# Kernel tuning notes

Measured on AMD Instinct MI355X. Metric: run time of the kernel, lower is better.

## Reference

```python
import jax, jax.numpy as jnp
import numpy as np

B, S, D, H = 8, 1024, 512, 8
HD = D // H
EPS = 1e-5


def layer_norm(x, g, b):
    m = jnp.mean(x, axis=-1, keepdims=True)
    v = jnp.mean(jnp.square(x - m), axis=-1, keepdims=True)
    return (x - m) * jax.lax.rsqrt(v + EPS) * g + b


def mha(x, w_in, b_in, w_out, b_out):
    # x: [B,S,D]; w_in: [3D,D]; PyTorch MultiheadAttention math (no dropout, eval)
    b, s, d = x.shape
    qkv = x @ w_in.T + b_in                      # [B,S,3D]
    q, k, v = jnp.split(qkv, 3, axis=-1)
    q = q.reshape(b, s, H, HD)
    k = k.reshape(b, s, H, HD)
    v = v.reshape(b, s, H, HD)
    scores = jnp.einsum('bqhd,bkhd->bhqk', q, k) / np.sqrt(HD)
    a = jax.nn.softmax(scores, axis=-1)
    o = jnp.einsum('bhqk,bkhd->bqhd', a, v).reshape(b, s, d)
    return o @ w_out.T + b_out


def interp_linear(y, out_size):
    # y: [B,S_in,D]; torch F.interpolate(mode='linear', align_corners=False)
    s_in = y.shape[1]
    scale = s_in / out_size
    src = (jnp.arange(out_size, dtype=jnp.float32) + 0.5) * scale - 0.5
    src = jnp.clip(src, 0.0, s_in - 1.0)
    i0 = jnp.floor(src).astype(jnp.int32)
    i1 = jnp.minimum(i0 + 1, s_in - 1)
    w = (src - i0.astype(jnp.float32))[None, :, None]
    return y[:, i0, :] * (1.0 - w) + y[:, i1, :] * w


def setup_inputs() -> dict:
    key = jax.random.key(0)
    ks = jax.random.split(key, 16)
    sd = 0.02
    return {
        'x': jax.random.normal(ks[0], (B, S, D), jnp.float32),
        'w_in1': jax.random.normal(ks[1], (3 * D, D), jnp.float32) * sd,
        'b_in1': jnp.zeros((3 * D,), jnp.float32),
        'w_out1': jax.random.normal(ks[2], (D, D), jnp.float32) * sd,
        'b_out1': jnp.zeros((D,), jnp.float32),
        'w_in2': jax.random.normal(ks[3], (3 * D, D), jnp.float32) * sd,
        'b_in2': jnp.zeros((3 * D,), jnp.float32),
        'w_out2': jax.random.normal(ks[4], (D, D), jnp.float32) * sd,
        'b_out2': jnp.zeros((D,), jnp.float32),
        'g1': jnp.ones((D,), jnp.float32), 'beta1': jnp.zeros((D,), jnp.float32),
        'g2': jnp.ones((D,), jnp.float32), 'beta2': jnp.zeros((D,), jnp.float32),
        'g3': jnp.ones((D,), jnp.float32), 'beta3': jnp.zeros((D,), jnp.float32),
        'w_ff1': jax.random.normal(ks[5], (4 * D, D), jnp.float32) * sd,
        'b_ff1': jnp.zeros((4 * D,), jnp.float32),
        'w_ff2': jax.random.normal(ks[6], (D, 4 * D), jnp.float32) * sd,
        'b_ff2': jnp.zeros((D,), jnp.float32),
    }


def reference(x, w_in1, b_in1, w_out1, b_out1, w_in2, b_in2, w_out2, b_out2,
              g1, beta1, g2, beta2, g3, beta3, w_ff1, b_ff1, w_ff2, b_ff2):
    a1 = mha(x, w_in1, b_in1, w_out1, b_out1)
    x = layer_norm(x + a1, g1, beta1)
    # avg_pool1d kernel=2 stride=2 ceil_mode (S even -> exact halving)
    pooled = x.reshape(B, S // 2, 2, D).mean(axis=2)
    a2 = mha(pooled, w_in2, b_in2, w_out2, b_out2)
    up = interp_linear(a2, S)
    x = layer_norm(x + up, g2, beta2)
    h = jax.nn.gelu(x @ w_ff1.T + b_ff1, approximate=False)
    ff = h @ w_ff2.T + b_ff2
    return layer_norm(x + ff, g3, beta3)
```

## Files before the change

### kernel.cpp

```cpp
#include <hip/hip_runtime.h>
#include <hip/hip_bf16.h>
#include <math.h>

typedef __hip_bfloat16 bf16;
typedef __attribute__((ext_vector_type(8))) short short8;
typedef __attribute__((ext_vector_type(4))) short s4v;
typedef __attribute__((ext_vector_type(4))) float f32x4;

__device__ __forceinline__ float ldf(const float* p, size_t i) { return p[i]; }
__device__ __forceinline__ float ldf(const bf16*  p, size_t i) { return __bfloat162float(p[i]); }
__device__ __forceinline__ void  stf(float* p, size_t i, float v) { p[i] = v; }
__device__ __forceinline__ void  stf(bf16*  p, size_t i, float v) { p[i] = __float2bfloat16(v); }

__device__ __forceinline__ float ex2(float x) { return __builtin_amdgcn_exp2f(x); }

__device__ __forceinline__ void gl16(const void* gp, void* lp) {
    __builtin_amdgcn_global_load_lds(
        (const __attribute__((address_space(1))) void*)gp,
        (__attribute__((address_space(3))) void*)lp, 16, 0, 0);
}

__global__ __launch_bounds__(256) void cvt_kernel(
    const float* __restrict__ src, bf16* __restrict__ dst, int n)
{
    for (int i = blockIdx.x * 256 + threadIdx.x; i < n; i += gridDim.x * 256)
        dst[i] = __float2bfloat16(src[i]);
}

__global__ __launch_bounds__(256) void cvt_w(
    const float* __restrict__ s0, const float* __restrict__ s1,
    const float* __restrict__ s2, const float* __restrict__ s3,
    const float* __restrict__ s4, const float* __restrict__ s5,
    bf16* __restrict__ dst)
{
    int i = blockIdx.x * 256 + threadIdx.x;
    const float* s; int off;
    if      (i <  786432) { s = s0; off = 0; }
    else if (i < 1048576) { s = s1; off =  786432; }
    else if (i < 1835008) { s = s2; off = 1048576; }
    else if (i < 2097152) { s = s3; off = 1835008; }
    else if (i < 3145728) { s = s4; off = 2097152; }
    else                  { s = s5; off = 3145728; }
    dst[i] = __float2bfloat16(s[i - off]);
}

template <int EPI>
__global__ __launch_bounds__(256) void gemm_mfma(
    const bf16* __restrict__ A, const bf16* __restrict__ W,
    const float* __restrict__ bias, bf16* __restrict__ C,
    int M, int N, int K)
{
    __shared__ __align__(16) bf16 Asl[2][128 * 64];
    __shared__ __align__(16) bf16 Bsl[2][128 * 64];

    const int tid  = threadIdx.x;
    const int lane = tid & 63;
    const int wave = tid >> 6;
    const int wm   = wave >> 1;
    const int wn   = wave & 1;
    const int l15  = lane & 15;
    const int quad = lane >> 4;
    const int sr   = lane >> 3;
    const int sc   = ((lane & 7) ^ sr) * 8;

    const int row0 = blockIdx.y * 128, col0 = blockIdx.x * 128;

    f32x4 acc[4][4] = {};

    const int nk = K >> 6;

    #pragma unroll
    for (int t = 0; t < 4; t++) {
        int r0 = wave * 32 + t * 8;
        gl16(&A[(size_t)(row0 + r0 + sr) * K + sc], &Asl[0][r0 * 64]);
        gl16(&W[(size_t)(col0 + r0 + sr) * K + sc], &Bsl[0][r0 * 64]);
    }

    int cur = 0;
    for (int i = 0; i < nk; i++) {
        __syncthreads();
        if (i + 1 < nk) {
            int k1 = (i + 1) << 6;
            #pragma unroll
            for (int t = 0; t < 4; t++) {
                int r0 = wave * 32 + t * 8;
                gl16(&A[(size_t)(row0 + r0 + sr) * K + k1 + sc], &Asl[cur ^ 1][r0 * 64]);
                gl16(&W[(size_t)(col0 + r0 + sr) * K + k1 + sc], &Bsl[cur ^ 1][r0 * 64]);
            }
        }

        #pragma unroll
        for (int ks = 0; ks < 64; ks += 32) {
            short8 af[4], bfr[4];
            const int g0 = (ks >> 3) + quad;
            const int col = (g0 ^ (l15 & 7)) * 8;
            #pragma unroll
            for (int mt = 0; mt < 4; mt++)
                af[mt] = *(const short8*)&Asl[cur][(wm * 64 + mt * 16 + l15) * 64 + col];
            #pragma unroll
            for (int nt = 0; nt < 4; nt++)
                bfr[nt] = *(const short8*)&Bsl[cur][(wn * 64 + nt * 16 + l15) * 64 + col];
            #pragma unroll
            for (int mt = 0; mt < 4; mt++)
                #pragma unroll
                for (int nt = 0; nt < 4; nt++)
                    acc[mt][nt] = __builtin_amdgcn_mfma_f32_16x16x32_bf16(
                        af[mt], bfr[nt], acc[mt][nt], 0, 0, 0);
        }
        cur ^= 1;
    }

    #pragma unroll
    for (int mt = 0; mt < 4; mt++) {
        int row = row0 + wm * 64 + mt * 16 + quad * 4;
        #pragma unroll
        for (int nt = 0; nt < 4; nt++) {
            int col = col0 + wn * 64 + nt * 16 + l15;
            float bv = bias[col];
            #pragma unroll
            for (int r = 0; r < 4; r++) {
                float v = acc[mt][nt][r] + bv;
                if (EPI == 1) v = 0.5f * v * (1.0f + erff(v * 0.70710678118654752f));
                C[(size_t)(row + r) * N + col] = __float2bfloat16(v);
            }
        }
    }
}

template <int LQ>
__global__ __launch_bounds__(256) void flash_attn_mfma(
    const bf16* __restrict__ qkv, bf16* __restrict__ o)
{
    __shared__ __align__(16) bf16 Ks[64 * 72];
    __shared__ __align__(16) bf16 Vt[64 * 68];
    __shared__ __align__(16) bf16 Pl[4][16 * 72];

    const int S   = 64 << LQ;
    const int nQB = 1 << LQ;

    const int tid  = threadIdx.x;
    const int wave = tid >> 6, lane = tid & 63;
    const int l15  = lane & 15, quad = lane >> 4;

    const int r    = blockIdx.x;
    const int w    = (r & 7) * (8 << LQ) + (r >> 3);
    const int qblk = w & (nQB - 1);
    const int bh   = w >> LQ;
    const int h    = bh & 7, bb = bh >> 3;
    const int q0   = qblk * 64;

    const bf16* base = qkv + (size_t)bb * S * 1536 + h * 64;

    short8 qf[2];
    {
        size_t qoff = (size_t)(q0 + wave * 16 + l15) * 1536;
        qf[0] = *(const short8*)&base[qoff + quad * 8];
        qf[1] = *(const short8*)&base[qoff + 32 + quad * 8];
    }

    f32x4 oacc[4] = {};
    float m2 = -3.0e38f, lrow = 0.f;
    const float CE = 0.18033688f;

    short8 kst[2];
    s4v    vst[4];
    const int vr4 = (tid >> 4) * 4;
    const int vc0 = (tid & 15) * 4;

    auto LOADK = [&](int k0) {
        #pragma unroll
        for (int t = 0; t < 2; t++) {
            int c = tid + 256 * t;
            int rr = c >> 3, col = (c & 7) * 8;
            kst[t] = *(const short8*)&base[(size_t)(k0 + rr) * 1536 + 512 + col];
        }
        #pragma unroll
        for (int rr = 0; rr < 4; rr++)
            vst[rr] = *(const s4v*)&base[(size_t)(k0 + vr4 + rr) * 1536 + 1024 + vc0];
    };

    auto WRITEKV = [&]() {
        #pragma unroll
        for (int t = 0; t < 2; t++) {
            int c = tid + 256 * t;
            int rr = c >> 3, col = (c & 7) * 8;
            *(short8*)&Ks[rr * 72 + col] = kst[t];
        }
        #pragma unroll
        for (int i = 0; i < 4; i++) {
            union { bf16 b[4]; unsigned u[2]; } pk;
            pk.b[0] = ((const bf16*)&vst[0])[i];
            pk.b[1] = ((const bf16*)&vst[1])[i];
            pk.b[2] = ((const bf16*)&vst[2])[i];
            pk.b[3] = ((const bf16*)&vst[3])[i];
            *(unsigned long long*)&Vt[(vc0 + i) * 68 + vr4] =
                *(const unsigned long long*)pk.u;
        }
    };

    LOADK(0);
    const int nt = 1 << LQ;
    for (int it = 0; it < nt; it++) {
        __syncthreads();
        WRITEKV();
        __syncthreads();
        if (it + 1 < nt) LOADK((it + 1) << 6);

        f32x4 st[4] = {};
        #pragma unroll
        for (int mt = 0; mt < 4; mt++) {
            short8 kf0 = *(const short8*)&Ks[(mt * 16 + l15) * 72 + quad * 8];
            short8 kf1 = *(const short8*)&Ks[(mt * 16 + l15) * 72 + 32 + quad * 8];
            st[mt] = __builtin_amdgcn_mfma_f32_16x16x32_bf16(kf0, qf[0], st[mt], 0, 0, 0);
            st[mt] = __builtin_amdgcn_mfma_f32_16x16x32_bf16(kf1, qf[1], st[mt], 0, 0, 0);
        }

        float cm = -3.0e38f;
        #pragma unroll
        for (int mt = 0; mt < 4; mt++)
            #pragma unroll
            for (int rr = 0; rr < 4; rr++) cm = fmaxf(cm, st[mt][rr]);
        cm = fmaxf(cm, __shfl_xor(cm, 16));
        cm = fmaxf(cm, __shfl_xor(cm, 32));
        float cm2 = cm * CE;

        if (__any(cm2 > m2 + 8.f)) {
            float mn2   = fmaxf(m2, cm2);
            float alpha = ex2(m2 - mn2);
            m2 = mn2;
            lrow *= alpha;
            float a4[4];
            #pragma unroll
            for (int rr = 0; rr < 4; rr++) a4[rr] = __shfl(alpha, quad * 4 + rr);
            #pragma unroll
            for (int ntt = 0; ntt < 4; ntt++)
                #pragma unroll
                for (int rr = 0; rr < 4; rr++) oacc[ntt][rr] *= a4[rr];
        }

        float ps = 0.f;
        #pragma unroll
        for (int mt = 0; mt < 4; mt++) {
            s4v pw;
            #pragma unroll
            for (int rr = 0; rr < 4; rr++) {
                float p = ex2(st[mt][rr] * CE - m2);
                ps += p;
                union { bf16 b; short hh; } cv;
                cv.b = __float2bfloat16(p);
                pw[rr] = cv.hh;
            }
            *(s4v*)&Pl[wave][l15 * 72 + mt * 16 + quad * 4] = pw;
        }
        ps += __shfl_xor(ps, 16);
        ps += __shfl_xor(ps, 32);
        lrow += ps;

        #pragma unroll
        for (int kb = 0; kb < 2; kb++) {
            short8 pf = *(const short8*)&Pl[wave][l15 * 72 + kb * 32 + quad * 8];
            #pragma unroll
            for (int ntt = 0; ntt < 4; ntt++) {
                const bf16* vp = &Vt[(ntt * 16 + l15) * 68 + kb * 32 + quad * 8];
                short8 vf;
                *(unsigned long long*)&vf       = *(const unsigned long long*)vp;
                *((unsigned long long*)&vf + 1) = *(const unsigned long long*)(vp + 4);
                oacc[ntt] = __builtin_amdgcn_mfma_f32_16x16x32_bf16(pf, vf, oacc[ntt], 0, 0, 0);
            }
        }
    }

    float inv = 1.0f / lrow;
    float iv[4];
    #pragma unroll
    for (int rr = 0; rr < 4; rr++) iv[rr] = __shfl(inv, quad * 4 + rr);
    #pragma unroll
    for (int ntt = 0; ntt < 4; ntt++)
        #pragma unroll
        for (int rr = 0; rr < 4; rr++) {
            size_t row = (size_t)bb * S + q0 + wave * 16 + quad * 4 + rr;
            o[row * 512 + h * 64 + ntt * 16 + l15] = __float2bfloat16(oacc[ntt][rr] * iv[rr]);
        }
}

template <typename AT, typename OT, bool INTERP>
__global__ __launch_bounds__(256) void ln_kernel(
    const AT* __restrict__ a, const bf16* __restrict__ bsrc,
    const float* __restrict__ g, const float* __restrict__ beta,
    OT* __restrict__ out)
{
    const int row = blockIdx.x;
    const int t = threadIdx.x;
    const size_t base = (size_t)row * 512;

    float a0 = ldf(a, base + t), a1 = ldf(a, base + t + 256);
    float b0, b1;
    if (INTERP) {
        int s = row & 1023, bb = row >> 10;
        float src = fminf(fmaxf((s + 0.5f) * 0.5f - 0.5f, 0.f), 511.f);
        int i0 = (int)src;
        int i1 = min(i0 + 1, 511);
        float w = src - (float)i0;
        size_t r0 = ((size_t)bb * 512 + i0) * 512;
        size_t r1 = ((size_t)bb * 512 + i1) * 512;
        b0 = __bfloat162float(bsrc[r0 + t]) * (1.f - w) + __bfloat162float(bsrc[r1 + t]) * w;
        b1 = __bfloat162float(bsrc[r0 + t + 256]) * (1.f - w) + __bfloat162float(bsrc[r1 + t + 256]) * w;
    } else {
        b0 = __bfloat162float(bsrc[base + t]);
        b1 = __bfloat162float(bsrc[base + t + 256]);
    }
    float v0 = a0 + b0, v1 = a1 + b1;

    __shared__ float red[4];
    const int lane = t & 63, wid = t >> 6;

    float sm = v0 + v1;
    #pragma unroll
    for (int off = 32; off > 0; off >>= 1) sm += __shfl_xor(sm, off);
    if (lane == 0) red[wid] = sm;
    __syncthreads();
    sm = red[0] + red[1] + red[2] + red[3];
    const float mean = sm * (1.0f / 512.0f);

    float d0 = v0 - mean, d1 = v1 - mean;
    float vv = d0 * d0 + d1 * d1;
    __syncthreads();
    #pragma unroll
    for (int off = 32; off > 0; off >>= 1) vv += __shfl_xor(vv, off);
    if (lane == 0) red[wid] = vv;
    __syncthreads();
    vv = red[0] + red[1] + red[2] + red[3];
    const float rstd = rsqrtf(vv * (1.0f / 512.0f) + 1e-5f);

    stf(out, base + t,       d0 * rstd * g[t]       + beta[t]);
    stf(out, base + t + 256, d1 * rstd * g[t + 256] + beta[t + 256]);
}

__global__ __launch_bounds__(256) void pool_kernel(
    const bf16* __restrict__ x, bf16* __restrict__ p)
{
    size_t i = (size_t)blockIdx.x * 256 + threadIdx.x;
    size_t d = i & 511;
    size_t rs = i >> 9;
    size_t b = rs >> 9, s = rs & 511;
    size_t r = (b * 1024 + 2 * s) * 512 + d;
    p[i] = __float2bfloat16(0.5f * (__bfloat162float(x[r]) + __bfloat162float(x[r + 512])));
}

extern "C" void kernel_launch(void* const* d_in, const int* in_sizes, int n_in,
                              void* d_out, int out_size, void* d_ws, size_t ws_size,
                              hipStream_t stream)
{
    const float* x      = (const float*)d_in[0];
    const float* w_in1  = (const float*)d_in[1];
    const float* b_in1  = (const float*)d_in[2];
    const float* w_out1 = (const float*)d_in[3];
    const float* b_out1 = (const float*)d_in[4];
    const float* w_in2  = (const float*)d_in[5];
    const float* b_in2  = (const float*)d_in[6];
    const float* w_out2 = (const float*)d_in[7];
    const float* b_out2 = (const float*)d_in[8];
    const float* g1     = (const float*)d_in[9];
    const float* be1    = (const float*)d_in[10];
    const float* g2     = (const float*)d_in[11];
    const float* be2    = (const float*)d_in[12];
    const float* g3     = (const float*)d_in[13];
    const float* be3    = (const float*)d_in[14];
    const float* w_ff1  = (const float*)d_in[15];
    const float* b_ff1  = (const float*)d_in[16];
    const float* w_ff2  = (const float*)d_in[17];
    const float* b_ff2  = (const float*)d_in[18];

    bf16* ws     = (bf16*)d_ws;
    bf16* xb     = ws + 0;
    bf16* wq1    = ws + 4194304;
    bf16* wo1    = ws + 4980736;
    bf16* wq2    = ws + 5242880;
    bf16* wo2    = ws + 6029312;
    bf16* wf1    = ws + 6291456;
    bf16* wf2    = ws + 7340032;
    bf16* qkv1   = ws + 8388608;
    bf16* o1     = ws + 20971520;
    bf16* a1     = ws + 25165824;
    bf16* x1     = ws + 29360128;
    bf16* pooled = ws + 33554432;
    bf16* qkv2   = ws + 35651584;
    bf16* o2     = ws + 41943040;
    bf16* a2     = ws + 44040192;
    bf16* x2     = ws + 46137344;
    bf16* h      = ws + 8388608;
    bf16* ff     = ws + 25165824;

    dim3 blk(256);

    cvt_kernel<<<4096, blk, 0, stream>>>(x, xb, 4194304);
    cvt_w<<<16384, blk, 0, stream>>>(w_in1, w_out1, w_in2, w_out2, w_ff1, w_ff2, wq1);

    gemm_mfma<0><<<dim3(12, 64), blk, 0, stream>>>(xb, wq1, b_in1, qkv1, 8192, 1536, 512);
    flash_attn_mfma<4><<<dim3(1024), blk, 0, stream>>>(qkv1, o1);
    gemm_mfma<0><<<dim3(4, 64), blk, 0, stream>>>(o1, wo1, b_out1, a1, 8192, 512, 512);
    ln_kernel<float, bf16, false><<<8192, blk, 0, stream>>>(x, a1, g1, be1, x1);
    pool_kernel<<<8192, blk, 0, stream>>>(x1, pooled);
    gemm_mfma<0><<<dim3(12, 32), blk, 0, stream>>>(pooled, wq2, b_in2, qkv2, 4096, 1536, 512);
    flash_attn_mfma<3><<<dim3(512), blk, 0, stream>>>(qkv2, o2);
    gemm_mfma<0><<<dim3(4, 32), blk, 0, stream>>>(o2, wo2, b_out2, a2, 4096, 512, 512);
    ln_kernel<bf16, bf16, true><<<8192, blk, 0, stream>>>(x1, a2, g2, be2, x2);
    gemm_mfma<1><<<dim3(16, 64), blk, 0, stream>>>(x2, wf1, b_ff1, h, 8192, 2048, 512);
    gemm_mfma<0><<<dim3(4, 64), blk, 0, stream>>>(h, wf2, b_ff2, ff, 8192, 512, 2048);
    ln_kernel<bf16, float, false><<<8192, blk, 0, stream>>>(x2, ff, g3, be3, (float*)d_out);
}
```

Baseline: 338.1 us.

## Rewrite flash attention with 32x32 MFMA, register-resident P and swizzled LDS

The attention kernel moves from 16x16x32 to 32x32x16 bf16 MFMA, with 2 waves of 32 query rows each per 128-thread block. The P matrix stays in registers, packed with v_cvt_pk_bf16_f32 and rearranged with v_permlane32_swap instead of a round trip through LDS. K and V tiles use an XOR-swizzled LDS layout to avoid bank conflicts. This cuts LDS traffic and instruction count per tile, at the cost of more registers per thread and fewer threads to cooperate on each KV load.

```diff
diff --git a/kernel.cpp b/kernel.cpp
--- a/kernel.cpp
+++ b/kernel.cpp
@@ -6,6 +6,7 @@
 typedef __attribute__((ext_vector_type(8))) short short8;
 typedef __attribute__((ext_vector_type(4))) short s4v;
 typedef __attribute__((ext_vector_type(4))) float f32x4;
+typedef __attribute__((ext_vector_type(16))) float f32x16;
 
 __device__ __forceinline__ float ldf(const float* p, size_t i) { return p[i]; }
 __device__ __forceinline__ float ldf(const bf16*  p, size_t i) { return __bfloat162float(p[i]); }
@@ -18,6 +19,14 @@
     __builtin_amdgcn_global_load_lds(
         (const __attribute__((address_space(1))) void*)gp,
         (__attribute__((address_space(3))) void*)lp, 16, 0, 0);
+}
+
+__device__ __forceinline__ int lof(int row, int bo) {
+    return row * 136 + (((bo >> 4) ^ (row & 7)) << 4) + (bo & 15);
+}
+
+__device__ __forceinline__ void pl32swap(unsigned &a, unsigned &b) {
+    asm volatile("v_permlane32_swap_b32 %0, %1" : "+v"(a), "+v"(b));
 }
 
 __global__ __launch_bounds__(256) void cvt_kernel(
@@ -127,160 +136,150 @@
     }
 }
 
-template <int LQ>
-__global__ __launch_bounds__(256) void flash_attn_mfma(
+template <int LQB>
+__global__ __launch_bounds__(128) void flash_attn_mfma(
     const bf16* __restrict__ qkv, bf16* __restrict__ o)
 {
-    __shared__ __align__(16) bf16 Ks[64 * 72];
+    constexpr int S  = 64 << LQB;
+    constexpr int nt = 1 << LQB;
+
+    __shared__ __align__(16) bf16 Kl[64 * 68];
     __shared__ __align__(16) bf16 Vt[64 * 68];
-    __shared__ __align__(16) bf16 Pl[4][16 * 72];
-
-    const int S   = 64 << LQ;
-    const int nQB = 1 << LQ;
+    __shared__ float aB[2][32];
 
     const int tid  = threadIdx.x;
     const int wave = tid >> 6, lane = tid & 63;
-    const int l15  = lane & 15, quad = lane >> 4;
+    const int l31  = lane & 31, hi = lane >> 5;
 
     const int r    = blockIdx.x;
-    const int w    = (r & 7) * (8 << LQ) + (r >> 3);
-    const int qblk = w & (nQB - 1);
-    const int bh   = w >> LQ;
+    const int w    = (r & 7) * ((1 << LQB) * 8) + (r >> 3);
+    const int qblk = w & ((1 << LQB) - 1);
+    const int bh   = w >> LQB;
     const int h    = bh & 7, bb = bh >> 3;
-    const int q0   = qblk * 64;
+    const int q0   = qblk * 64 + wave * 32;
 
     const bf16* base = qkv + (size_t)bb * S * 1536 + h * 64;
-
-    short8 qf[2];
-    {
-        size_t qoff = (size_t)(q0 + wave * 16 + l15) * 1536;
-        qf[0] = *(const short8*)&base[qoff + quad * 8];
-        qf[1] = *(const short8*)&base[qoff + 32 + quad * 8];
-    }
-
-    f32x4 oacc[4] = {};
+    char* Kb = (char*)Kl;
+    char* Vb = (char*)Vt;
+
+    short8 qf[4];
+    #pragma unroll
+    for (int c = 0; c < 4; c++)
+        qf[c] = *(const short8*)&base[(size_t)(q0 + l31) * 1536 + c * 16 + hi * 8];
+
+    f32x16 oacc[2] = {};
     float m2 = -3.0e38f, lrow = 0.f;
     const float CE = 0.18033688f;
 
-    short8 kst[2];
-    s4v    vst[4];
-    const int vr4 = (tid >> 4) * 4;
-    const int vc0 = (tid & 15) * 4;
-
-    auto LOADK = [&](int k0) {
-        #pragma unroll
-        for (int t = 0; t < 2; t++) {
-            int c = tid + 256 * t;
-            int rr = c >> 3, col = (c & 7) * 8;
-            kst[t] = *(const short8*)&base[(size_t)(k0 + rr) * 1536 + 512 + col];
-        }
-        #pragma unroll
-        for (int rr = 0; rr < 4; rr++)
-            vst[rr] = *(const s4v*)&base[(size_t)(k0 + vr4 + rr) * 1536 + 1024 + vc0];
+    const int kr  = tid >> 1, kh = tid & 1;
+    const int vc0 = (tid & 15) * 4, vr8 = (tid >> 4) * 8;
+
+    short8 kst[4];
+    s4v    vst[8];
+
+    auto LOADKV = [&](int k0) {
+        #pragma unroll
+        for (int i = 0; i < 4; i++)
+            kst[i] = *(const short8*)&base[(size_t)(k0 + kr) * 1536 + 512 + kh * 32 + i * 8];
+        #pragma unroll
+        for (int i = 0; i < 8; i++)
+            vst[i] = *(const s4v*)&base[(size_t)(k0 + vr8 + i) * 1536 + 1024 + vc0];
     };
 
     auto WRITEKV = [&]() {
         #pragma unroll
-        for (int t = 0; t < 2; t++) {
-            int c = tid + 256 * t;
-            int rr = c >> 3, col = (c & 7) * 8;
-            *(short8*)&Ks[rr * 72 + col] = kst[t];
-        }
-        #pragma unroll
         for (int i = 0; i < 4; i++) {
-            union { bf16 b[4]; unsigned u[2]; } pk;
-            pk.b[0] = ((const bf16*)&vst[0])[i];
-            pk.b[1] = ((const bf16*)&vst[1])[i];
-            pk.b[2] = ((const bf16*)&vst[2])[i];
-            pk.b[3] = ((const bf16*)&vst[3])[i];
-            *(unsigned long long*)&Vt[(vc0 + i) * 68 + vr4] =
-                *(const unsigned long long*)pk.u;
+            int off = lof(kr, kh * 64 + i * 16);
+            *(long*)(Kb + off)     = ((const long*)&kst[i])[0];
+            *(long*)(Kb + off + 8) = ((const long*)&kst[i])[1];
+        }
+        #pragma unroll
+        for (int i = 0; i < 4; i++) {
+            union { bf16 b[8]; long l[2]; } pk;
+            #pragma unroll
+            for (int j = 0; j < 8; j++) pk.b[j] = ((const bf16*)&vst[j])[i];
+            int off = lof(vc0 + i, vr8 * 2);
+            *(long*)(Vb + off)     = pk.l[0];
+            *(long*)(Vb + off + 8) = pk.l[1];
         }
     };
 
-    LOADK(0);
-    const int nt = 1 << LQ;
+    LOADKV(0);
     for (int it = 0; it < nt; it++) {
         __syncthreads();
         WRITEKV();
         __syncthreads();
-        if (it + 1 < nt) LOADK((it + 1) << 6);
-
-        f32x4 st[4] = {};
-        #pragma unroll
-        for (int mt = 0; mt < 4; mt++) {
-            short8 kf0 = *(const short8*)&Ks[(mt * 16 + l15) * 72 + quad * 8];
-            short8 kf1 = *(const short8*)&Ks[(mt * 16 + l15) * 72 + 32 + quad * 8];
-            st[mt] = __builtin_amdgcn_mfma_f32_16x16x32_bf16(kf0, qf[0], st[mt], 0, 0, 0);
-            st[mt] = __builtin_amdgcn_mfma_f32_16x16x32_bf16(kf1, qf[1], st[mt], 0, 0, 0);
-        }
-
-        float cm = -3.0e38f;
-        #pragma unroll
-        for (int mt = 0; mt < 4; mt++)
-            #pragma unroll
-            for (int rr = 0; rr < 4; rr++) cm = fmaxf(cm, st[mt][rr]);
-        cm = fmaxf(cm, __shfl_xor(cm, 16));
-        cm = fmaxf(cm, __shfl_xor(cm, 32));
-        float cm2 = cm * CE;
-
-        if (__any(cm2 > m2 + 8.f)) {
-            float mn2   = fmaxf(m2, cm2);
-            float alpha = ex2(m2 - mn2);
-            m2 = mn2;
-            lrow *= alpha;
-            float a4[4];
-            #pragma unroll
-            for (int rr = 0; rr < 4; rr++) a4[rr] = __shfl(alpha, quad * 4 + rr);
-            #pragma unroll
-            for (int ntt = 0; ntt < 4; ntt++)
+        if (it + 1 < nt) LOADKV((it + 1) << 6);
+
+        #pragma unroll
+        for (int sub = 0; sub < 2; sub++) {
+            f32x16 st = {};
+            #pragma unroll
+            for (int c = 0; c < 4; c++) {
+                union { long l[2]; short8 s; } af;
+                int off = lof(sub * 32 + l31, c * 32 + hi * 16);
+                af.l[0] = *(const long*)(Kb + off);
+                af.l[1] = *(const long*)(Kb + off + 8);
+                st = __builtin_amdgcn_mfma_f32_32x32x16_bf16(af.s, qf[c], st, 0, 0, 0);
+            }
+
+            float cm = st[0];
+            #pragma unroll
+            for (int r2 = 1; r2 < 16; r2++) cm = fmaxf(cm, st[r2]);
+            cm = fmaxf(cm, __shfl_xor(cm, 32));
+            float cm2 = cm * CE;
+
+            if (__any(cm2 > m2 + 8.f)) {
+                float mn2 = fmaxf(m2, cm2);
+                float alpha = ex2(m2 - mn2);
+                m2 = mn2; lrow *= alpha;
+                if (hi == 0) aB[wave][l31] = alpha;
                 #pragma unroll
-                for (int rr = 0; rr < 4; rr++) oacc[ntt][rr] *= a4[rr];
-        }
-
-        float ps = 0.f;
-        #pragma unroll
-        for (int mt = 0; mt < 4; mt++) {
-            s4v pw;
-            #pragma unroll
-            for (int rr = 0; rr < 4; rr++) {
-                float p = ex2(st[mt][rr] * CE - m2);
-                ps += p;
-                union { bf16 b; short hh; } cv;
-                cv.b = __float2bfloat16(p);
-                pw[rr] = cv.hh;
+                for (int r2 = 0; r2 < 16; r2++) {
+                    float av = aB[wave][(r2 & 3) + 8 * (r2 >> 2) + 4 * hi];
+                    oacc[0][r2] *= av; oacc[1][r2] *= av;
+                }
             }
-            *(s4v*)&Pl[wave][l15 * 72 + mt * 16 + quad * 4] = pw;
-        }
-        ps += __shfl_xor(ps, 16);
-        ps += __shfl_xor(ps, 32);
-        lrow += ps;
-
-        #pragma unroll
-        for (int kb = 0; kb < 2; kb++) {
-            short8 pf = *(const short8*)&Pl[wave][l15 * 72 + kb * 32 + quad * 8];
-            #pragma unroll
-            for (int ntt = 0; ntt < 4; ntt++) {
-                const bf16* vp = &Vt[(ntt * 16 + l15) * 68 + kb * 32 + quad * 8];
-                short8 vf;
-                *(unsigned long long*)&vf       = *(const unsigned long long*)vp;
-                *((unsigned long long*)&vf + 1) = *(const unsigned long long*)(vp + 4);
-                oacc[ntt] = __builtin_amdgcn_mfma_f32_16x16x32_bf16(pf, vf, oacc[ntt], 0, 0, 0);
+
+            float p[16]; float ps = 0.f;
+            #pragma unroll
+            for (int r2 = 0; r2 < 16; r2++) { p[r2] = ex2(st[r2] * CE - m2); ps += p[r2]; }
+            ps += __shfl_xor(ps, 32);
+            lrow += ps;
+
+            unsigned wk[8];
+            #pragma unroll
+            for (int j = 0; j < 8; j++)
+                asm("v_cvt_pk_bf16_f32 %0, %1, %2" : "=v"(wk[j]) : "v"(p[2*j]), "v"(p[2*j+1]));
+
+            #pragma unroll
+            for (int kk = 0; kk < 2; kk++) {
+                pl32swap(wk[kk*4+0], wk[kk*4+2]);
+                pl32swap(wk[kk*4+1], wk[kk*4+3]);
+                union { unsigned u[4]; short8 s; } pa;
+                pa.u[0] = wk[kk*4+0]; pa.u[1] = wk[kk*4+1];
+                pa.u[2] = wk[kk*4+2]; pa.u[3] = wk[kk*4+3];
+                #pragma unroll
+                for (int dt = 0; dt < 2; dt++) {
+                    union { long l[2]; short8 s; } vf;
+                    int off = lof(dt * 32 + l31, sub * 64 + kk * 32 + hi * 16);
+                    vf.l[0] = *(const long*)(Vb + off);
+                    vf.l[1] = *(const long*)(Vb + off + 8);
+                    oacc[dt] = __builtin_amdgcn_mfma_f32_32x32x16_bf16(pa.s, vf.s, oacc[dt], 0, 0, 0);
+                }
             }
         }
     }
 
-    float inv = 1.0f / lrow;
-    float iv[4];
-    #pragma unroll
-    for (int rr = 0; rr < 4; rr++) iv[rr] = __shfl(inv, quad * 4 + rr);
-    #pragma unroll
-    for (int ntt = 0; ntt < 4; ntt++)
-        #pragma unroll
-        for (int rr = 0; rr < 4; rr++) {
-            size_t row = (size_t)bb * S + q0 + wave * 16 + quad * 4 + rr;
-            o[row * 512 + h * 64 + ntt * 16 + l15] = __float2bfloat16(oacc[ntt][rr] * iv[rr]);
-        }
+    if (hi == 0) aB[wave][l31] = 1.0f / lrow;
+    #pragma unroll
+    for (int r2 = 0; r2 < 16; r2++) {
+        int qr = (r2 & 3) + 8 * (r2 >> 2) + 4 * hi;
+        float iv = aB[wave][qr];
+        size_t rb = ((size_t)bb * S + q0 + qr) * 512 + h * 64;
+        o[rb + l31]      = __float2bfloat16(oacc[0][r2] * iv);
+        o[rb + 32 + l31] = __float2bfloat16(oacc[1][r2] * iv);
+    }
 }
 
 template <typename AT, typename OT, bool INTERP>
@@ -392,17 +391,18 @@
     bf16* ff     = ws + 25165824;
 
     dim3 blk(256);
+    dim3 fblk(128);
 
     cvt_kernel<<<4096, blk, 0, stream>>>(x, xb, 4194304);
     cvt_w<<<16384, blk, 0, stream>>>(w_in1, w_out1, w_in2, w_out2, w_ff1, w_ff2, wq1);
 
     gemm_mfma<0><<<dim3(12, 64), blk, 0, stream>>>(xb, wq1, b_in1, qkv1, 8192, 1536, 512);
-    flash_attn_mfma<4><<<dim3(1024), blk, 0, stream>>>(qkv1, o1);
+    flash_attn_mfma<4><<<dim3(1024), fblk, 0, stream>>>(qkv1, o1);
     gemm_mfma<0><<<dim3(4, 64), blk, 0, stream>>>(o1, wo1, b_out1, a1, 8192, 512, 512);
     ln_kernel<float, bf16, false><<<8192, blk, 0, stream>>>(x, a1, g1, be1, x1);
     pool_kernel<<<8192, blk, 0, stream>>>(x1, pooled);
     gemm_mfma<0><<<dim3(12, 32), blk, 0, stream>>>(pooled, wq2, b_in2, qkv2, 4096, 1536, 512);
-    flash_attn_mfma<3><<<dim3(512), blk, 0, stream>>>(qkv2, o2);
+    flash_attn_mfma<3><<<dim3(512), fblk, 0, stream>>>(qkv2, o2);
     gemm_mfma<0><<<dim3(4, 32), blk, 0, stream>>>(o2, wo2, b_out2, a2, 4096, 512, 512);
     ln_kernel<bf16, bf16, true><<<8192, blk, 0, stream>>>(x1, a2, g2, be2, x2);
     gemm_mfma<1><<<dim3(16, 64), blk, 0, stream>>>(x2, wf1, b_ff1, h, 8192, 2048, 512);
```

New measurement: 337.3 us. Within noise of the previous version (-0.3%).
